# Kernel optimization log

Hardware: AMD Instinct MI355X
Metric: run time of the kernel (lower is better)

The kernel has to match this reference:

```python
import jax, jax.numpy as jnp
import numpy as np

EPS = 1e-5
KH = KW = 3
PAD = 1

def conv3x3(x, w, b=None):
    out = jax.lax.conv_general_dilated(
        x, w, window_strides=(1, 1), padding=((PAD, PAD), (PAD, PAD)),
        dimension_numbers=("NCHW", "OIHW", "NCHW"))
    if b is not None:
        out = out + b[None, :, None, None]
    return out

def batchnorm(x, gamma, beta):
    # training-mode BatchNorm2d: batch statistics over (N, H, W)
    mean = x.mean(axis=(0, 2, 3), keepdims=True)
    var = x.var(axis=(0, 2, 3), keepdims=True)
    return gamma[None, :, None, None] * (x - mean) / jnp.sqrt(var + EPS) + beta[None, :, None, None]

def bilinear_gather(x, y_pos, x_pos):
    # x: [B,C,H,W]; y_pos/x_pos: [B,P,H,W] (P = KH*KW sampling taps)
    # zero padding outside image (mmcv modulated deform conv semantics)
    B, C, H, W = x.shape
    P = y_pos.shape[1]
    x_flat = x.reshape(B, C, H * W)
    y0 = jnp.floor(y_pos)
    x0 = jnp.floor(x_pos)
    ly = y_pos - y0
    lx = x_pos - x0
    out = jnp.zeros((B, C, P, H, W), dtype=x.dtype)
    for dy, dx, wgt in ((0, 0, (1 - ly) * (1 - lx)), (0, 1, (1 - ly) * lx),
                        (1, 0, ly * (1 - lx)), (1, 1, ly * lx)):
        yi = y0 + dy
        xi = x0 + dx
        valid = ((yi >= 0) & (yi <= H - 1) & (xi >= 0) & (xi <= W - 1)).astype(x.dtype)
        yc = jnp.clip(yi, 0, H - 1).astype(jnp.int32)
        xc = jnp.clip(xi, 0, W - 1).astype(jnp.int32)
        idx = (yc * W + xc).reshape(B, 1, P * H * W)
        vals = jnp.take_along_axis(x_flat, jnp.broadcast_to(idx, (B, C, P * H * W)), axis=2)
        vals = vals.reshape(B, C, P, H, W)
        out = out + vals * (wgt * valid)[:, None]
    return out  # [B,C,P,H,W]

def modulated_deform_conv(x, w_off, b_off, w_dcn):
    B, C, H, W = x.shape
    P = KH * KW
    off = conv3x3(x, w_off, b_off)  # [B, 3*P, H, W]
    o1, o2, m = jnp.split(off, 3, axis=1)
    offset = jnp.concatenate([o1, o2], axis=1)            # [B, 2P, H, W]
    offset = offset.reshape(B, P, 2, H, W)                # channel 2p -> dy, 2p+1 -> dx
    mask = jax.nn.sigmoid(m)                              # [B, P, H, W]
    hh = jnp.arange(H, dtype=x.dtype)
    ww = jnp.arange(W, dtype=x.dtype)
    ky = jnp.arange(KH, dtype=x.dtype)
    kx = jnp.arange(KW, dtype=x.dtype)
    # base sampling grid per tap p = ky*KW + kx: (h - PAD + ky, w - PAD + kx)
    base_y = (hh[None, :] - PAD + ky[:, None])            # [KH, H]
    base_x = (ww[None, :] - PAD + kx[:, None])            # [KW, W]
    base_y = jnp.broadcast_to(base_y[:, None, :, None], (KH, KW, H, W)).reshape(P, H, W)
    base_x = jnp.broadcast_to(base_x[None, :, None, :], (KH, KW, H, W)).reshape(P, H, W)
    y_pos = base_y[None] + offset[:, :, 0]                # [B,P,H,W]
    x_pos = base_x[None] + offset[:, :, 1]
    sampled = bilinear_gather(x, y_pos, x_pos)            # [B,C,P,H,W]
    sampled = sampled * mask[:, None]
    w = w_dcn.reshape(w_dcn.shape[0], C, P)               # [O, C, P]
    return jnp.einsum("bcphw,ocp->bohw", sampled, w)

def setup_inputs() -> dict:
    key = jax.random.key(0)
    ks = jax.random.split(key, 10)
    B, Ch, H, W = 4, 256, 64, 64
    Cin, Cout = 2 * Ch, 256
    P = KH * KW
    inp = {
        "input_v": jax.random.normal(ks[0], (B, Ch, H, W), jnp.float32),
        "input_i": jax.random.normal(ks[1], (B, Ch, H, W), jnp.float32),
        "w_off": jax.random.normal(ks[2], (3 * P, Cin, KH, KW), jnp.float32) * 0.01,
        "b_off": jnp.zeros((3 * P,), jnp.float32),
        "w_dcn": jax.random.normal(ks[3], (Cout, Cin, KH, KW), jnp.float32) * (1.0 / np.sqrt(Cin * P)),
        "gamma1": jnp.ones((Cout,), jnp.float32),
        "beta1": jnp.zeros((Cout,), jnp.float32),
        "w2": jax.random.normal(ks[4], (Cout, Cout, KH, KW), jnp.float32) * (1.0 / np.sqrt(Cout * P)),
        "gamma2": jnp.ones((Cout,), jnp.float32),
        "beta2": jnp.zeros((Cout,), jnp.float32),
    }
    return inp

def reference(input_v, input_i, w_off, b_off, w_dcn, gamma1, beta1, w2, gamma2, beta2):
    x = jnp.concatenate([input_v, input_i], axis=1)
    out = modulated_deform_conv(x, w_off, b_off, w_dcn)
    out = jax.nn.relu(batchnorm(out, gamma1, beta1))
    out = jax.nn.relu(batchnorm(conv3x3(out, w2), gamma2, beta2))
    return out
```

## Files before the change

### kernel.cpp

```cpp
#include <hip/hip_runtime.h>
#include <cstdint>
#include <cstddef>

typedef unsigned short u16;
typedef __attribute__((ext_vector_type(8))) short s16x8;
typedef __attribute__((ext_vector_type(4))) float f32x4;

#define DEV __device__ __forceinline__

DEV float bf2f(short u){
  union { unsigned int i; float f; } v;
  v.i = ((unsigned int)(u16)u) << 16;
  return v.f;
}
DEV short f2bf(float f){
  union { float f; unsigned int i; } v; v.f = f;
  unsigned int u = v.i;
  u += 0x7fffu + ((u >> 16) & 1u);
  return (short)(u >> 16);
}
DEV f32x4 f32x4_zero(){
  f32x4 z;
#pragma unroll
  for(int j=0;j<4;j++) z[j]=0.f;
  return z;
}
DEV f32x4 mfma16(s16x8 a, s16x8 b, f32x4 c){
  return __builtin_amdgcn_mfma_f32_16x16x32_bf16(a, b, c, 0, 0, 0);
}
DEV void cp16(const void* g, void* l){
  __builtin_amdgcn_global_load_lds(
      (const __attribute__((address_space(1))) unsigned int*)g,
      (__attribute__((address_space(3))) unsigned int*)l, 16, 0, 0);
}

static constexpr size_t OFF_ACC_B   = 0;
static constexpr size_t OUT1_ACC_B  = 2097152;
static constexpr size_t OUT2_ACC_B  = 18874368;
static constexpr size_t STATS_B     = 35651584;
static constexpr size_t ZERO_BYTES  = 35655680;
static constexpr size_t XN_PAD_B    = 35655680;
static constexpr size_t OUT1N_PAD_B = 53497856;
static constexpr size_t WOFFT_B     = 62418944;
static constexpr size_t WDCNT_B     = 62713856;
static constexpr size_t W2T_B       = 65073152;
static constexpr size_t SAMP_O_B    = 66252800;
static constexpr size_t SAMP_W_B    = 68612096;

__global__ void k_border(u16* __restrict__ xp, u16* __restrict__ op){
  const int cid = blockIdx.x, t = threadIdx.x;
  const int b = cid / 260, rem = cid % 260;
  int y, x;
  if(rem < 132){ y = (rem/66)*65; x = rem%66; }
  else { int r2 = rem-132; x = (r2>>6)*65; y = 1 + (r2&63); }
  const size_t cell = (size_t)(b*66+y)*66 + x;
  ((unsigned int*)(xp + cell*512))[t] = 0;
  if(t < 128) ((unsigned int*)(op + cell*256))[t] = 0;
}

__global__ void k_x_to_nhwc(const float* __restrict__ v, const float* __restrict__ vi,
                            u16* __restrict__ xn){
  __shared__ float tile[64][65];
  const int b = blockIdx.z, c0 = blockIdx.y*64, h = blockIdx.x;
  const float* src = (c0 < 256) ? (v  + ((size_t)b*256 + c0)      *4096)
                                : (vi + ((size_t)b*256 + (c0-256))*4096);
  const int t = threadIdx.x;
#pragma unroll
  for(int k=0;k<16;k++){
    int idx = t + k*256;
    int cl = idx >> 6, wl = idx & 63;
    tile[cl][wl] = src[(size_t)cl*4096 + h*64 + wl];
  }
  __syncthreads();
#pragma unroll
  for(int k=0;k<16;k++){
    int idx = t + k*256;
    int wl = idx >> 6, cl = idx & 63;
    xn[((size_t)(b*66 + h+1)*66 + (wl+1))*512 + c0 + cl] = (u16)f2bf(tile[cl][wl]);
  }
}

__global__ void k_prep_woff(const float* __restrict__ w, u16* __restrict__ wt){
  int i = blockIdx.x*256 + threadIdx.x;
  if(i >= 147456) return;
  int j = i & 7, n = (i>>3) & 31, kcp = i>>8;
  int kc = kcp & 63, tp = kcp >> 6;
  int c = kc*8 + j;
  float val = (n < 27) ? w[(size_t)(n*512 + c)*9 + tp] : 0.f;
  wt[i] = (u16)f2bf(val);
}
__global__ void k_prep_wdcn(const float* __restrict__ w, u16* __restrict__ wt){
  int i = blockIdx.x*256 + threadIdx.x;
  if(i >= 1179648) return;
  int j = i & 7, n = (i>>3) & 255, kcp = i>>11;
  int kc = kcp & 63, tp = kcp >> 6;
  int c = kc*8 + j;
  wt[i] = (u16)f2bf(w[(size_t)(n*512 + c)*9 + tp]);
}
__global__ void k_prep_w2(const float* __restrict__ w, u16* __restrict__ wt){
  int i = blockIdx.x*256 + threadIdx.x;
  if(i >= 589824) return;
  int j = i & 7, n = (i>>3) & 255, kcp = i>>11;
  int kc = kcp & 31, tp = kcp >> 5;
  int c = kc*8 + j;
  wt[i] = (u16)f2bf(w[(size_t)(n*256 + c)*9 + tp]);
}

__global__ __launch_bounds__(256, 6) void k_conv_off(
    const u16* __restrict__ xn, const u16* __restrict__ wt, float* __restrict__ offa){
  __shared__ short A[2][4][64][8];
  __shared__ short B[2][4][32][8];
  const int tid = threadIdx.x;
  const int lane = tid & 63, wid = tid >> 6;
  const int quad = lane >> 4, ln = lane & 15;
  const int m0 = blockIdx.x * 64;
  const int b = m0 >> 12, h = (m0 >> 6) & 63;
  const int gst0 = blockIdx.y * 24;
  const int m_base = wid * 16;
  f32x4 acc0 = f32x4_zero(), acc1 = f32x4_zero();

  {
    const int tp = gst0 >> 4, s = gst0 & 15;
    const int ty = tp/3, tx = tp - ty*3;
    cp16(xn + ((size_t)(b*66 + h+ty)*66 + lane + tx)*512 + s*32 + wid*8, &A[0][wid][0][0]);
    if(wid < 2)
      cp16(wt + ((size_t)tp*64 + s*4)*256 + wid*512 + lane*8, (short*)&B[0][0][0][0] + wid*512);
  }
  __syncthreads();

  int buf = 0;
  for(int it=0; it<24; it++){
    const int nb = buf ^ 1;
    if(it < 23){
      const int gn = gst0 + it + 1;
      const int tp = gn >> 4, s = gn & 15;
      const int ty = tp/3, tx = tp - ty*3;
      cp16(xn + ((size_t)(b*66 + h+ty)*66 + lane + tx)*512 + s*32 + wid*8, &A[nb][wid][0][0]);
      if(wid < 2)
        cp16(wt + ((size_t)tp*64 + s*4)*256 + wid*512 + lane*8, (short*)&B[nb][0][0][0] + wid*512);
    }
    const s16x8* Ap = (const s16x8*)&A[buf][0][0][0];
    const s16x8* Bp = (const s16x8*)&B[buf][0][0][0];
    s16x8 a  = Ap[quad*64 + m_base + ln];
    s16x8 b0 = Bp[quad*32 + ln];
    s16x8 b1 = Bp[quad*32 + 16 + ln];
    acc0 = mfma16(a, b0, acc0);
    acc1 = mfma16(a, b1, acc1);
    __syncthreads();
    buf = nb;
  }
#pragma unroll
  for(int nf=0;nf<2;nf++){
    const f32x4 v = nf ? acc1 : acc0;
    const int col = nf*16 + ln;
#pragma unroll
    for(int i=0;i<4;i++){
      const int row = m_base + quad*4 + i;
      unsafeAtomicAdd(offa + (size_t)(m0+row)*32 + col, v[i]);
    }
  }
}

__global__ void k_sampler(const float* __restrict__ offa, const float* __restrict__ boff,
                          int* __restrict__ so, float* __restrict__ sw){
  const int idx = blockIdx.x*256 + threadIdx.x;
  if(idx >= 16384*9) return;
  const int m = idx / 9, tp = idx - m*9;
  const int b = m >> 12, h = (m >> 6) & 63, w = m & 63;
  const float* orow = offa + (size_t)m*32;
  float dy = orow[2*tp]   + boff[2*tp];
  float dx = orow[2*tp+1] + boff[2*tp+1];
  float mz = orow[18+tp]  + boff[18+tp];
  float mk = 1.f / (1.f + expf(-mz));
  float ypos = (float)(h - 1 + tp/3) + dy;
  float xpos = (float)(w - 1 + tp%3) + dx;
  float y0f = floorf(ypos), x0f = floorf(xpos);
  float ly = ypos - y0f, lx = xpos - x0f;
  int y0 = (int)y0f, x0 = (int)x0f;
#pragma unroll
  for(int k=0;k<4;k++){
    int ddy = k >> 1, ddx = k & 1;
    int yi = y0 + ddy, xi = x0 + ddx;
    bool vv = (yi >= 0) & (yi < 64) & (xi >= 0) & (xi < 64);
    float wk = (ddy ? ly : 1.f-ly) * (ddx ? lx : 1.f-lx) * mk;
    if(!vv) wk = 0.f;
    int yc = yi < 0 ? 0 : (yi > 63 ? 63 : yi);
    int xc = xi < 0 ? 0 : (xi > 63 ? 63 : xi);
    so[(size_t)idx*4 + k] = ((b*66 + yc+1)*66 + xc+1) << 9;
    sw[(size_t)idx*4 + k] = wk;
  }
}

__global__ __launch_bounds__(256, 4) void k_dcn(
    const u16* __restrict__ xn, const u16* __restrict__ wt,
    const int* __restrict__ so, const float* __restrict__ sw,
    float* __restrict__ outa){
  __shared__ short A[2][4][64][8];
  __shared__ short B[2][4][256][8];
  const int tid = threadIdx.x;
  const int lane = tid & 63, wid = tid >> 6;
  const int quad = lane >> 4, ln = lane & 15;
  const int m0 = blockIdx.x * 64;
  const int gst0 = blockIdx.y * 24;
  const int m_base = (wid >> 1)*32, n_base = (wid & 1)*128;
  const int r = tid >> 2, sub = tid & 3;
  f32x4 acc[2][8];
#pragma unroll
  for(int mf=0;mf<2;mf++)
#pragma unroll
    for(int nf=0;nf<8;nf++) acc[mf][nf] = f32x4_zero();

  int4 po; float4 pw;
  s16x8 g0, g1, g2, g3;

  {
    const int tp = gst0 >> 4, s = gst0 & 15;
    po = *(const int4*)  (so + ((size_t)(m0+r)*9 + tp)*4);
    pw = *(const float4*)(sw + ((size_t)(m0+r)*9 + tp)*4);
    const u16* bs = wt + ((size_t)tp*64 + s*4)*2048 + (wid*4)*512 + lane*8;
    short* bd = (short*)&B[0][0][0][0] + (wid*4)*512;
#pragma unroll
    for(int i=0;i<4;i++) cp16(bs + i*512, bd + i*512);
    const int c0 = s*32 + sub*8;
    g0 = *(const s16x8*)(xn + po.x + c0);
    g1 = *(const s16x8*)(xn + po.y + c0);
    g2 = *(const s16x8*)(xn + po.z + c0);
    g3 = *(const s16x8*)(xn + po.w + c0);
    s16x8 pk;
#pragma unroll
    for(int j=0;j<8;j++){
      float f = pw.x * bf2f(g0[j]);
      f = fmaf(pw.y, bf2f(g1[j]), f);
      f = fmaf(pw.z, bf2f(g2[j]), f);
      f = fmaf(pw.w, bf2f(g3[j]), f);
      pk[j] = f2bf(f);
    }
    *(s16x8*)(&A[0][sub][r][0]) = pk;
  }
  __syncthreads();

  int buf = 0;
  for(int it=0; it<24; it++){
    const int nb = buf ^ 1;
    if(it < 23){
      const int gn = gst0 + it + 1;
      const int tp = gn >> 4, s = gn & 15;
      if((gn & 15) == 0){
        po = *(const int4*)  (so + ((size_t)(m0+r)*9 + tp)*4);
        pw = *(const float4*)(sw + ((size_t)(m0+r)*9 + tp)*4);
      }
      const u16* bs = wt + ((size_t)tp*64 + s*4)*2048 + (wid*4)*512 + lane*8;
      short* bd = (short*)&B[nb][0][0][0] + (wid*4)*512;
#pragma unroll
      for(int i=0;i<4;i++) cp16(bs + i*512, bd + i*512);
      const int c0 = s*32 + sub*8;
      g0 = *(const s16x8*)(xn + po.x + c0);
      g1 = *(const s16x8*)(xn + po.y + c0);
      g2 = *(const s16x8*)(xn + po.z + c0);
      g3 = *(const s16x8*)(xn + po.w + c0);
    }
    {
      const s16x8* Ap = (const s16x8*)&A[buf][0][0][0];
      const s16x8* Bp = (const s16x8*)&B[buf][0][0][0];
      s16x8 a0 = Ap[quad*64 + m_base + ln];
      s16x8 a1 = Ap[quad*64 + m_base + 16 + ln];
#pragma unroll
      for(int nf=0;nf<8;nf++){
        s16x8 bf = Bp[quad*256 + n_base + nf*16 + ln];
        acc[0][nf] = mfma16(a0, bf, acc[0][nf]);
        acc[1][nf] = mfma16(a1, bf, acc[1][nf]);
      }
    }
    if(it < 23){
      s16x8 pk;
#pragma unroll
      for(int j=0;j<8;j++){
        float f = pw.x * bf2f(g0[j]);
        f = fmaf(pw.y, bf2f(g1[j]), f);
        f = fmaf(pw.z, bf2f(g2[j]), f);
        f = fmaf(pw.w, bf2f(g3[j]), f);
        pk[j] = f2bf(f);
      }
      *(s16x8*)(&A[nb][sub][r][0]) = pk;
    }
    __syncthreads();
    buf = nb;
  }
#pragma unroll
  for(int mf=0;mf<2;mf++)
#pragma unroll
    for(int nf=0;nf<8;nf++){
      const int col = n_base + nf*16 + ln;
#pragma unroll
      for(int i=0;i<4;i++){
        const int row = m_base + mf*16 + quad*4 + i;
        unsafeAtomicAdd(outa + (size_t)(m0+row)*256 + col, acc[mf][nf][i]);
      }
    }
}

__global__ __launch_bounds__(256, 4) void k_conv2(
    const u16* __restrict__ a_in, const u16* __restrict__ wt, float* __restrict__ outa){
  __shared__ short A[2][4][64][8];
  __shared__ short B[2][4][256][8];
  const int tid = threadIdx.x;
  const int lane = tid & 63, wid = tid >> 6;
  const int quad = lane >> 4, ln = lane & 15;
  const int m0 = blockIdx.x * 64;
  const int b = m0 >> 12, h = (m0 >> 6) & 63;
  const int gst0 = blockIdx.y * 12;
  const int m_base = (wid >> 1)*32, n_base = (wid & 1)*128;
  f32x4 acc[2][8];
#pragma unroll
  for(int mf=0;mf<2;mf++)
#pragma unroll
    for(int nf=0;nf<8;nf++) acc[mf][nf] = f32x4_zero();

  {
    const int tp = gst0 >> 3, s = gst0 & 7;
    const int ty = tp/3, tx = tp - ty*3;
    cp16(a_in + ((size_t)(b*66 + h+ty)*66 + lane + tx)*256 + s*32 + wid*8, &A[0][wid][0][0]);
    const u16* bs = wt + ((size_t)tp*32 + s*4)*2048 + (wid*4)*512 + lane*8;
    short* bd = (short*)&B[0][0][0][0] + (wid*4)*512;
#pragma unroll
    for(int i=0;i<4;i++) cp16(bs + i*512, bd + i*512);
  }
  __syncthreads();

  int buf = 0;
  for(int it=0; it<12; it++){
    const int nb = buf ^ 1;
    if(it < 11){
      const int gn = gst0 + it + 1;
      const int tp = gn >> 3, s = gn & 7;
      const int ty = tp/3, tx = tp - ty*3;
      cp16(a_in + ((size_t)(b*66 + h+ty)*66 + lane + tx)*256 + s*32 + wid*8, &A[nb][wid][0][0]);
      const u16* bs = wt + ((size_t)tp*32 + s*4)*2048 + (wid*4)*512 + lane*8;
      short* bd = (short*)&B[nb][0][0][0] + (wid*4)*512;
#pragma unroll
      for(int i=0;i<4;i++) cp16(bs + i*512, bd + i*512);
    }
    const s16x8* Ap = (const s16x8*)&A[buf][0][0][0];
    const s16x8* Bp = (const s16x8*)&B[buf][0][0][0];
    s16x8 a0 = Ap[quad*64 + m_base + ln];
    s16x8 a1 = Ap[quad*64 + m_base + 16 + ln];
#pragma unroll
    for(int nf=0;nf<8;nf++){
      s16x8 bf = Bp[quad*256 + n_base + nf*16 + ln];
      acc[0][nf] = mfma16(a0, bf, acc[0][nf]);
      acc[1][nf] = mfma16(a1, bf, acc[1][nf]);
    }
    __syncthreads();
    buf = nb;
  }
#pragma unroll
  for(int mf=0;mf<2;mf++)
#pragma unroll
    for(int nf=0;nf<8;nf++){
      const int col = n_base + nf*16 + ln;
#pragma unroll
      for(int i=0;i<4;i++){
        const int row = m_base + mf*16 + quad*4 + i;
        unsafeAtomicAdd(outa + (size_t)(m0+row)*256 + col, acc[mf][nf][i]);
      }
    }
}

__global__ void k_stats(const float* __restrict__ acc, float* __restrict__ sum,
                        float* __restrict__ sq){
  const int m0 = blockIdx.x*64;
  const int c = threadIdx.x;
  float s = 0.f, q = 0.f;
  for(int i=0;i<64;i++){
    float v = acc[(size_t)(m0+i)*256 + c];
    s += v; q += v*v;
  }
  unsafeAtomicAdd(sum + c, s);
  unsafeAtomicAdd(sq + c, q);
}

__global__ void k_bn1(const float* __restrict__ acc, const float* __restrict__ sum,
                      const float* __restrict__ sq, const float* __restrict__ g,
                      const float* __restrict__ bt, u16* __restrict__ o){
  __shared__ float sc[256], sh[256];
  const int t = threadIdx.x;
  {
    float mean = sum[t] * (1.f/16384.f);
    float var  = sq[t] * (1.f/16384.f) - mean*mean;
    float rstd = rsqrtf(var + 1e-5f);
    float s = g[t] * rstd;
    sc[t] = s; sh[t] = bt[t] - mean*s;
  }
  __syncthreads();
  const int c4 = (t & 63) * 4;
  const float s0 = sc[c4], s1 = sc[c4+1], s2 = sc[c4+2], s3 = sc[c4+3];
  const float h0 = sh[c4], h1 = sh[c4+1], h2 = sh[c4+2], h3 = sh[c4+3];
#pragma unroll
  for(int k=0;k<4;k++){
    int m = blockIdx.x*16 + k*4 + (t>>6);
    int b = m >> 12, hh = (m >> 6) & 63, ww = m & 63;
    const float4 v = *(const float4*)(acc + (size_t)m*256 + c4);
    unsigned int lo = (unsigned int)(u16)f2bf(fmaxf(0.f, v.x*s0 + h0))
                    | ((unsigned int)(u16)f2bf(fmaxf(0.f, v.y*s1 + h1)) << 16);
    unsigned int hi = (unsigned int)(u16)f2bf(fmaxf(0.f, v.z*s2 + h2))
                    | ((unsigned int)(u16)f2bf(fmaxf(0.f, v.w*s3 + h3)) << 16);
    uint2 pr; pr.x = lo; pr.y = hi;
    *(uint2*)(o + ((size_t)(b*66 + hh+1)*66 + ww+1)*256 + c4) = pr;
  }
}

__global__ void k_bn2_out(const float* __restrict__ acc, const float* __restrict__ sum,
                          const float* __restrict__ sq, const float* __restrict__ g,
                          const float* __restrict__ bt, float* __restrict__ out){
  __shared__ float tile[64][65];
  __shared__ float sc[64], sh[64];
  const int t = threadIdx.x;
  const int b = blockIdx.z, c0 = blockIdx.y*64, hw0 = blockIdx.x*64;
  if(t < 64){
    int c = c0 + t;
    float mean = sum[c] * (1.f/16384.f);
    float var  = sq[c] * (1.f/16384.f) - mean*mean;
    float rstd = rsqrtf(var + 1e-5f);
    float s = g[c] * rstd;
    sc[t] = s; sh[t] = bt[c] - mean*s;
  }
  __syncthreads();
#pragma unroll
  for(int k=0;k<16;k++){
    int idx = t + k*256;
    int wl = idx >> 6, cl = idx & 63;
    float v = acc[(size_t)((b<<12) + hw0 + wl)*256 + c0 + cl];
    tile[wl][cl] = fmaxf(0.f, v*sc[cl] + sh[cl]);
  }
  __syncthreads();
#pragma unroll
  for(int k=0;k<16;k++){
    int idx = t + k*256;
    int cl = idx >> 6, wl = idx & 63;
    out[(size_t)(b*256 + c0 + cl)*4096 + hw0 + wl] = tile[wl][cl];
  }
}

extern "C" void kernel_launch(void* const* d_in, const int* in_sizes, int n_in,
                              void* d_out, int out_size, void* d_ws, size_t ws_size,
                              hipStream_t stream){
  const float* in_v  = (const float*)d_in[0];
  const float* in_i  = (const float*)d_in[1];
  const float* w_off = (const float*)d_in[2];
  const float* b_off = (const float*)d_in[3];
  const float* w_dcn = (const float*)d_in[4];
  const float* g1    = (const float*)d_in[5];
  const float* bt1   = (const float*)d_in[6];
  const float* w2    = (const float*)d_in[7];
  const float* g2    = (const float*)d_in[8];
  const float* bt2   = (const float*)d_in[9];
  float* out = (float*)d_out;
  char* ws = (char*)d_ws;

  float* off_acc  = (float*)(ws + OFF_ACC_B);
  float* out1_acc = (float*)(ws + OUT1_ACC_B);
  float* out2_acc = (float*)(ws + OUT2_ACC_B);
  float* stats    = (float*)(ws + STATS_B);
  float* sum1 = stats,       *sq1 = stats + 256;
  float* sum2 = stats + 512, *sq2 = stats + 768;
  u16* xn_pad    = (u16*)(ws + XN_PAD_B);
  u16* out1n_pad = (u16*)(ws + OUT1N_PAD_B);
  u16* wofft = (u16*)(ws + WOFFT_B);
  u16* wdcnt = (u16*)(ws + WDCNT_B);
  u16* w2t   = (u16*)(ws + W2T_B);
  int*   samp_o = (int*)(ws + SAMP_O_B);
  float* samp_w = (float*)(ws + SAMP_W_B);

  hipMemsetAsync(ws, 0, ZERO_BYTES, stream);
  k_border<<<1040, 256, 0, stream>>>(xn_pad, out1n_pad);
  k_x_to_nhwc<<<dim3(64,8,4), 256, 0, stream>>>(in_v, in_i, xn_pad);
  k_prep_woff<<<576, 256, 0, stream>>>(w_off, wofft);
  k_prep_wdcn<<<4608, 256, 0, stream>>>(w_dcn, wdcnt);
  k_prep_w2<<<2304, 256, 0, stream>>>(w2, w2t);
  k_conv_off<<<dim3(256,6), 256, 0, stream>>>(xn_pad, wofft, off_acc);
  k_sampler<<<576, 256, 0, stream>>>(off_acc, b_off, samp_o, samp_w);
  k_dcn<<<dim3(256,6), 256, 0, stream>>>(xn_pad, wdcnt, samp_o, samp_w, out1_acc);
  k_stats<<<256, 256, 0, stream>>>(out1_acc, sum1, sq1);
  k_bn1<<<1024, 256, 0, stream>>>(out1_acc, sum1, sq1, g1, bt1, out1n_pad);
  k_conv2<<<dim3(256,6), 256, 0, stream>>>(out1n_pad, w2t, out2_acc);
  k_stats<<<256, 256, 0, stream>>>(out2_acc, sum2, sq2);
  k_bn2_out<<<dim3(64,4,4), 256, 0, stream>>>(out2_acc, sum2, sq2, g2, bt2, out);
}
```

Measured before the change: 407.5 us.

## Split deformable conv into explicit sampling pass and plain GEMM

The bilinear sampling that was fused into the DCN GEMM's A-tile producer moves into its own kernel, which writes a materialized bf16 im2col matrix (16384 x 4608). The GEMM then streams A tiles directly into LDS with async copies, and split-K drops from 6 to 3 for both the DCN and conv2 kernels, so there are fewer atomic adds. The aim is to take gather latency and VALU work off the MFMA loop. In exchange it adds about 150MB of extra global traffic and halves the grid size, which lowers parallelism.

New measurement: 393.1 us. 3.5% less time.

```diff
diff --git a/kernel.cpp b/kernel.cpp
--- a/kernel.cpp
+++ b/kernel.cpp
@@ -46,6 +46,7 @@
 static constexpr size_t W2T_B       = 65073152;
 static constexpr size_t SAMP_O_B    = 66252800;
 static constexpr size_t SAMP_W_B    = 68612096;
+static constexpr size_t A_SAMP_B    = 70971392;
 
 __global__ void k_border(u16* __restrict__ xp, u16* __restrict__ op){
   const int cid = blockIdx.x, t = threadIdx.x;
@@ -191,87 +192,28 @@
   }
 }
 
-__global__ __launch_bounds__(256, 4) void k_dcn(
-    const u16* __restrict__ xn, const u16* __restrict__ wt,
-    const int* __restrict__ so, const float* __restrict__ sw,
-    float* __restrict__ outa){
-  __shared__ short A[2][4][64][8];
-  __shared__ short B[2][4][256][8];
-  const int tid = threadIdx.x;
-  const int lane = tid & 63, wid = tid >> 6;
-  const int quad = lane >> 4, ln = lane & 15;
-  const int m0 = blockIdx.x * 64;
-  const int gst0 = blockIdx.y * 24;
-  const int m_base = (wid >> 1)*32, n_base = (wid & 1)*128;
-  const int r = tid >> 2, sub = tid & 3;
-  f32x4 acc[2][8];
-#pragma unroll
-  for(int mf=0;mf<2;mf++)
-#pragma unroll
-    for(int nf=0;nf<8;nf++) acc[mf][nf] = f32x4_zero();
-
-  int4 po; float4 pw;
-  s16x8 g0, g1, g2, g3;
-
-  {
-    const int tp = gst0 >> 4, s = gst0 & 15;
-    po = *(const int4*)  (so + ((size_t)(m0+r)*9 + tp)*4);
-    pw = *(const float4*)(sw + ((size_t)(m0+r)*9 + tp)*4);
-    const u16* bs = wt + ((size_t)tp*64 + s*4)*2048 + (wid*4)*512 + lane*8;
-    short* bd = (short*)&B[0][0][0][0] + (wid*4)*512;
-#pragma unroll
-    for(int i=0;i<4;i++) cp16(bs + i*512, bd + i*512);
-    const int c0 = s*32 + sub*8;
-    g0 = *(const s16x8*)(xn + po.x + c0);
-    g1 = *(const s16x8*)(xn + po.y + c0);
-    g2 = *(const s16x8*)(xn + po.z + c0);
-    g3 = *(const s16x8*)(xn + po.w + c0);
-    s16x8 pk;
-#pragma unroll
-    for(int j=0;j<8;j++){
-      float f = pw.x * bf2f(g0[j]);
-      f = fmaf(pw.y, bf2f(g1[j]), f);
-      f = fmaf(pw.z, bf2f(g2[j]), f);
-      f = fmaf(pw.w, bf2f(g3[j]), f);
-      pk[j] = f2bf(f);
-    }
-    *(s16x8*)(&A[0][sub][r][0]) = pk;
-  }
-  __syncthreads();
-
-  int buf = 0;
-  for(int it=0; it<24; it++){
-    const int nb = buf ^ 1;
-    if(it < 23){
-      const int gn = gst0 + it + 1;
-      const int tp = gn >> 4, s = gn & 15;
-      if((gn & 15) == 0){
-        po = *(const int4*)  (so + ((size_t)(m0+r)*9 + tp)*4);
-        pw = *(const float4*)(sw + ((size_t)(m0+r)*9 + tp)*4);
-      }
-      const u16* bs = wt + ((size_t)tp*64 + s*4)*2048 + (wid*4)*512 + lane*8;
-      short* bd = (short*)&B[nb][0][0][0] + (wid*4)*512;
-#pragma unroll
-      for(int i=0;i<4;i++) cp16(bs + i*512, bd + i*512);
-      const int c0 = s*32 + sub*8;
-      g0 = *(const s16x8*)(xn + po.x + c0);
-      g1 = *(const s16x8*)(xn + po.y + c0);
-      g2 = *(const s16x8*)(xn + po.z + c0);
-      g3 = *(const s16x8*)(xn + po.w + c0);
-    }
-    {
-      const s16x8* Ap = (const s16x8*)&A[buf][0][0][0];
-      const s16x8* Bp = (const s16x8*)&B[buf][0][0][0];
-      s16x8 a0 = Ap[quad*64 + m_base + ln];
-      s16x8 a1 = Ap[quad*64 + m_base + 16 + ln];
-#pragma unroll
-      for(int nf=0;nf<8;nf++){
-        s16x8 bf = Bp[quad*256 + n_base + nf*16 + ln];
-        acc[0][nf] = mfma16(a0, bf, acc[0][nf]);
-        acc[1][nf] = mfma16(a1, bf, acc[1][nf]);
-      }
-    }
-    if(it < 23){
+__global__ __launch_bounds__(256) void k_sample_a(
+    const u16* __restrict__ xn, const int* __restrict__ so, const float* __restrict__ sw,
+    u16* __restrict__ as){
+  const int blk = blockIdx.x;
+  const int pb = ((blk & 7) << 5) | (blk >> 3);
+  const int m = pb*64 + (threadIdx.x >> 2);
+  const int q = threadIdx.x & 3;
+  for(int tp=0; tp<9; tp++){
+    const int4   po = *(const int4*)  (so + ((size_t)m*9 + tp)*4);
+    const float4 pw = *(const float4*)(sw + ((size_t)m*9 + tp)*4);
+    const u16* x0 = xn + po.x + q*8;
+    const u16* x1 = xn + po.y + q*8;
+    const u16* x2 = xn + po.z + q*8;
+    const u16* x3 = xn + po.w + q*8;
+    u16* dst = as + (size_t)m*4608 + tp*512 + q*8;
+#pragma unroll 4
+    for(int u=0; u<16; u++){
+      const int c0 = u*32;
+      s16x8 g0 = *(const s16x8*)(x0 + c0);
+      s16x8 g1 = *(const s16x8*)(x1 + c0);
+      s16x8 g2 = *(const s16x8*)(x2 + c0);
+      s16x8 g3 = *(const s16x8*)(x3 + c0);
       s16x8 pk;
 #pragma unroll
       for(int j=0;j<8;j++){
@@ -281,7 +223,60 @@
         f = fmaf(pw.w, bf2f(g3[j]), f);
         pk[j] = f2bf(f);
       }
-      *(s16x8*)(&A[nb][sub][r][0]) = pk;
+      *(s16x8*)(dst + c0) = pk;
+    }
+  }
+}
+
+__global__ __launch_bounds__(256, 4) void k_dcn_gemm(
+    const u16* __restrict__ as, const u16* __restrict__ wt, float* __restrict__ outa){
+  __shared__ short A[2][4][64][8];
+  __shared__ short B[2][4][256][8];
+  const int tid = threadIdx.x;
+  const int lane = tid & 63, wid = tid >> 6;
+  const int quad = lane >> 4, ln = lane & 15;
+  const int m0 = blockIdx.x * 64;
+  const int gst0 = blockIdx.y * 48;
+  const int m_base = (wid >> 1)*32, n_base = (wid & 1)*128;
+  f32x4 acc[2][8];
+#pragma unroll
+  for(int mf=0;mf<2;mf++)
+#pragma unroll
+    for(int nf=0;nf<8;nf++) acc[mf][nf] = f32x4_zero();
+
+  const u16* arow = as + (size_t)(m0 + lane)*4608;
+
+  {
+    const int tp = gst0 >> 4, s = gst0 & 15;
+    cp16(arow + gst0*32 + wid*8, &A[0][wid][0][0]);
+    const u16* bs = wt + ((size_t)tp*64 + s*4)*2048 + (wid*4)*512 + lane*8;
+    short* bd = (short*)&B[0][0][0][0] + (wid*4)*512;
+#pragma unroll
+    for(int i=0;i<4;i++) cp16(bs + i*512, bd + i*512);
+  }
+  __syncthreads();
+
+  int buf = 0;
+  for(int it=0; it<48; it++){
+    const int nb = buf ^ 1;
+    if(it < 47){
+      const int gn = gst0 + it + 1;
+      const int tp = gn >> 4, s = gn & 15;
+      cp16(arow + gn*32 + wid*8, &A[nb][wid][0][0]);
+      const u16* bs = wt + ((size_t)tp*64 + s*4)*2048 + (wid*4)*512 + lane*8;
+      short* bd = (short*)&B[nb][0][0][0] + (wid*4)*512;
+#pragma unroll
+      for(int i=0;i<4;i++) cp16(bs + i*512, bd + i*512);
+    }
+    const s16x8* Ap = (const s16x8*)&A[buf][0][0][0];
+    const s16x8* Bp = (const s16x8*)&B[buf][0][0][0];
+    s16x8 a0 = Ap[quad*64 + m_base + ln];
+    s16x8 a1 = Ap[quad*64 + m_base + 16 + ln];
+#pragma unroll
+    for(int nf=0;nf<8;nf++){
+      s16x8 bf = Bp[quad*256 + n_base + nf*16 + ln];
+      acc[0][nf] = mfma16(a0, bf, acc[0][nf]);
+      acc[1][nf] = mfma16(a1, bf, acc[1][nf]);
     }
     __syncthreads();
     buf = nb;
@@ -308,7 +303,7 @@
   const int quad = lane >> 4, ln = lane & 15;
   const int m0 = blockIdx.x * 64;
   const int b = m0 >> 12, h = (m0 >> 6) & 63;
-  const int gst0 = blockIdx.y * 12;
+  const int gst0 = blockIdx.y * 24;
   const int m_base = (wid >> 1)*32, n_base = (wid & 1)*128;
   f32x4 acc[2][8];
 #pragma unroll
@@ -328,9 +323,9 @@
   __syncthreads();
 
   int buf = 0;
-  for(int it=0; it<12; it++){
+  for(int it=0; it<24; it++){
     const int nb = buf ^ 1;
-    if(it < 11){
+    if(it < 23){
       const int gn = gst0 + it + 1;
       const int tp = gn >> 3, s = gn & 7;
       const int ty = tp/3, tx = tp - ty*3;
@@ -470,6 +465,7 @@
   u16* w2t   = (u16*)(ws + W2T_B);
   int*   samp_o = (int*)(ws + SAMP_O_B);
   float* samp_w = (float*)(ws + SAMP_W_B);
+  u16* a_samp = (u16*)(ws + A_SAMP_B);
 
   hipMemsetAsync(ws, 0, ZERO_BYTES, stream);
   k_border<<<1040, 256, 0, stream>>>(xn_pad, out1n_pad);
@@ -479,10 +475,11 @@
   k_prep_w2<<<2304, 256, 0, stream>>>(w2, w2t);
   k_conv_off<<<dim3(256,6), 256, 0, stream>>>(xn_pad, wofft, off_acc);
   k_sampler<<<576, 256, 0, stream>>>(off_acc, b_off, samp_o, samp_w);
-  k_dcn<<<dim3(256,6), 256, 0, stream>>>(xn_pad, wdcnt, samp_o, samp_w, out1_acc);
+  k_sample_a<<<256, 256, 0, stream>>>(xn_pad, samp_o, samp_w, a_samp);
+  k_dcn_gemm<<<dim3(256,3), 256, 0, stream>>>(a_samp, wdcnt, out1_acc);
   k_stats<<<256, 256, 0, stream>>>(out1_acc, sum1, sq1);
   k_bn1<<<1024, 256, 0, stream>>>(out1_acc, sum1, sq1, g1, bt1, out1n_pad);
-  k_conv2<<<dim3(256,6), 256, 0, stream>>>(out1n_pad, w2t, out2_acc);
+  k_conv2<<<dim3(256,3), 256, 0, stream>>>(out1n_pad, w2t, out2_acc);
   k_stats<<<256, 256, 0, stream>>>(out2_acc, sum2, sq2);
   k_bn2_out<<<dim3(64,4,4), 256, 0, stream>>>(out2_acc, sum2, sq2, g2, bt2, out);
 }
```
